# Kernel tuning notes

Measured on AMD Instinct MI355X. Metric: run time of the kernel, lower is better.

## Reference

```python
import jax, jax.numpy as jnp
import numpy as np

HEADS, DQK, DV = 4, 128, 128
HH, WW = 32, 32
SCALE = DQK ** -0.5
EPS = 1e-5


def bn(x, g, b, m, v):
    # eval-mode BatchNorm2d over channel dim of NCHW
    inv = g * jax.lax.rsqrt(v + EPS)
    return x * inv[:, None, None] + (b - m * inv)[:, None, None]


def rel_to_abs(x):
    # x: (B, Nh, L, 2L-1) -> (B, Nh, L, L)
    B, Nh, L, _ = x.shape
    x = jnp.pad(x, ((0, 0), (0, 0), (0, 0), (0, 1)))
    fx = x.reshape(B, Nh, L * 2 * L)
    fx = jnp.pad(fx, ((0, 0), (0, 0), (0, L - 1)))
    fx = fx.reshape(B, Nh, L + 1, 2 * L - 1)
    return fx[:, :, :L, L - 1:]


def rel_logits_1d(q, rel_k):
    # q: (B, Nh, H, W, D); rel_k: (2W-1, D)
    B, Nh, H, W, D = q.shape
    r = jnp.einsum('bnhwd,rd->bnhwr', q, rel_k)
    r = rel_to_abs(r.reshape(B, Nh * H, W, 2 * W - 1))
    r = r.reshape(B, Nh, H, W, W)
    return jnp.broadcast_to(r[:, :, :, None], (B, Nh, H, H, W, W))


def pos_bias(q, rel_h, rel_w):
    # q: (B, Nh, H*W, D), already scaled
    B, Nh, L, D = q.shape
    q5 = q.reshape(B, Nh, HH, WW, D)
    rw = rel_logits_1d(q5, rel_w)                     # (B,N,H,Hx,W,W)
    rw = rw.transpose(0, 1, 2, 4, 3, 5).reshape(B, Nh, HH * WW, HH * WW)
    rh = rel_logits_1d(q5.transpose(0, 1, 3, 2, 4), rel_h)  # (B,N,W,Wx,H,H)
    rh = rh.transpose(0, 1, 4, 2, 5, 3).reshape(B, Nh, HH * WW, HH * WW)
    return rw + rh


def to_heads(x):
    # (B, Nh*d, H, W) -> (B, Nh, H*W, d)
    B, C, H, W = x.shape
    x = x.reshape(B, HEADS, C // HEADS, H, W)
    return x.transpose(0, 1, 3, 4, 2).reshape(B, HEADS, H * W, C // HEADS)


def mhsa(x, w_qk, w_v, rel_h, rel_w):
    B, C, H, W = x.shape
    qk = jnp.einsum('bchw,oc->bohw', x, w_qk)
    q, k = jnp.split(qk, 2, axis=1)
    v = jnp.einsum('bchw,oc->bohw', x, w_v)
    q, k, v = to_heads(q), to_heads(k), to_heads(v)
    q = q * SCALE
    logits = jnp.einsum('bnid,bnjd->bnij', q, k) + pos_bias(q, rel_h, rel_w)
    weights = jax.nn.softmax(logits, axis=-1)
    out = jnp.einsum('bnij,bnjd->bnid', weights, v)   # (B,Nh,HW,dv)
    out = out.reshape(B, HEADS, H, W, DV).transpose(0, 1, 4, 2, 3)
    return out.reshape(B, HEADS * DV, H, W)


def setup_inputs() -> dict:
    key = jax.random.key(0)
    ks = jax.random.split(key, 12)
    d = {
        'x': jax.random.normal(ks[0], (8, 512, HH, WW), jnp.float32),
        'w_qk': jax.random.normal(ks[1], (2 * HEADS * DQK, 512), jnp.float32) * 0.02,
        'w_v': jax.random.normal(ks[2], (HEADS * DV, 512), jnp.float32) * 0.02,
        'rel_h': jax.random.normal(ks[3], (2 * HH - 1, DQK), jnp.float32) * SCALE,
        'rel_w': jax.random.normal(ks[4], (2 * WW - 1, DQK), jnp.float32) * SCALE,
        'g1': jnp.ones((512,), jnp.float32),
        'b1': jnp.zeros((512,), jnp.float32),
        'm1': jax.random.normal(ks[5], (512,), jnp.float32) * 0.1,
        'v1': jax.random.uniform(ks[6], (512,), jnp.float32) + 0.5,
        'g2': jnp.ones((512,), jnp.float32),
        'b2': jnp.zeros((512,), jnp.float32),
        'm2': jax.random.normal(ks[7], (512,), jnp.float32) * 0.1,
        'v2': jax.random.uniform(ks[8], (512,), jnp.float32) + 0.5,
        'w_fc': jax.random.normal(ks[9], (512, 512, 3, 3), jnp.float32) * 0.02,
        'bias_fc': jnp.zeros((512,), jnp.float32),
    }
    return d


def reference(x, w_qk, w_v, rel_h, rel_w, g1, b1, m1, v1, g2, b2, m2, v2, w_fc, bias_fc):
    out = jax.nn.relu(bn(x, g1, b1, m1, v1))
    out = mhsa(out, w_qk, w_v, rel_h, rel_w)
    x = out + x
    out = jax.nn.relu(bn(x, g2, b2, m2, v2))
    out = jax.lax.conv_general_dilated(
        out, w_fc, window_strides=(1, 1), padding='SAME',
        dimension_numbers=('NCHW', 'OIHW', 'NCHW')) + bias_fc[:, None, None]
    return out + x
```

## Files before the change

### kernel.cpp

```cpp
#include <hip/hip_runtime.h>

typedef __bf16 v8bf __attribute__((ext_vector_type(8)));
typedef float f32x4 __attribute__((ext_vector_type(4)));

#define DEVI static __device__ __forceinline__

DEVI v8bf load8(const __bf16* p) { return *reinterpret_cast<const v8bf*>(p); }

DEVI f32x4 mfma16(v8bf a, v8bf b, f32x4 c) {
  return __builtin_amdgcn_mfma_f32_16x16x32_bf16(a, b, c, 0, 0, 0);
}

DEVI void gld16(const __bf16* g, __bf16* l) {
  __builtin_amdgcn_global_load_lds(
      (const __attribute__((address_space(1))) unsigned int*)(const void*)g,
      (__attribute__((address_space(3))) unsigned int*)(void*)l, 16, 0, 0);
}

#define SCALE_Q 0.08838834764831845f

__global__ void k_prep(const float* __restrict__ wqk, const float* __restrict__ wv,
                       const float* __restrict__ relh, const float* __restrict__ relw,
                       const float* __restrict__ wfc, __bf16* __restrict__ wqkb,
                       __bf16* __restrict__ wvb, __bf16* __restrict__ rhb,
                       __bf16* __restrict__ rwb, __bf16* __restrict__ Wt,
                       float* __restrict__ zpad4) {
  const int bid = blockIdx.x, tid = threadIdx.x;
  if (bid < 2048) {
    int i = bid * 256 + tid;
    wqkb[i] = (__bf16)wqk[i];
  } else if (bid < 3072) {
    int i = (bid - 2048) * 256 + tid;
    wvb[i] = (__bf16)wv[i];
  } else if (bid < 3104) {
    int i = (bid - 3072) * 256 + tid;
    if (i < 8064) rhb[i] = (__bf16)relh[i];
  } else if (bid < 3136) {
    int i = (bid - 3104) * 256 + tid;
    if (i < 8064) rwb[i] = (__bf16)relw[i];
  } else if (bid < 4160) {
    int i = (bid - 3136) * 256 + tid;
    const float* src = wfc + (size_t)i * 9;
#pragma unroll
    for (int tap = 0; tap < 9; ++tap)
      Wt[(size_t)tap * 262144 + i] = (__bf16)src[tap];
  } else {
    int i = (bid - 4160) * 256 + tid;
    f32x4 z = {0.f, 0.f, 0.f, 0.f};
    reinterpret_cast<f32x4*>(zpad4)[i] = z;
  }
}

__global__ void k_bn1(const float* __restrict__ x, const float* __restrict__ g,
                      const float* __restrict__ bb, const float* __restrict__ m,
                      const float* __restrict__ v, __bf16* __restrict__ y) {
  __shared__ float tile[32][33];
  const int b = blockIdx.z, c0 = blockIdx.y * 32, s0 = blockIdx.x * 32;
  const int tx = threadIdx.x, ty = threadIdx.y;
#pragma unroll
  for (int r = 0; r < 4; ++r) {
    int c = c0 + ty + r * 8;
    float inv = g[c] * rsqrtf(v[c] + 1e-5f);
    float beta = bb[c] - m[c] * inv;
    float val = x[((size_t)b * 512 + c) * 1024 + s0 + tx] * inv + beta;
    tile[ty + r * 8][tx] = fmaxf(val, 0.0f);
  }
  __syncthreads();
#pragma unroll
  for (int r = 0; r < 4; ++r) {
    int s = s0 + ty + r * 8;
    y[((size_t)b * 1024 + s) * 512 + c0 + tx] = (__bf16)tile[tx][ty + r * 8];
  }
}

__global__ void k_bn2(const float* __restrict__ x2, const float* __restrict__ g,
                      const float* __restrict__ bb, const float* __restrict__ m,
                      const float* __restrict__ v, __bf16* __restrict__ zp) {
  __shared__ float tile[32][33];
  const int b = blockIdx.z, c0 = blockIdx.y * 32, s0 = blockIdx.x * 32;
  const int tx = threadIdx.x, ty = threadIdx.y;
#pragma unroll
  for (int r = 0; r < 4; ++r) {
    int c = c0 + ty + r * 8;
    float inv = g[c] * rsqrtf(v[c] + 1e-5f);
    float beta = bb[c] - m[c] * inv;
    float val = x2[((size_t)b * 512 + c) * 1024 + s0 + tx] * inv + beta;
    tile[ty + r * 8][tx] = fmaxf(val, 0.0f);
  }
  __syncthreads();
#pragma unroll
  for (int r = 0; r < 4; ++r) {
    int s = s0 + ty + r * 8;
    int hh = s >> 5, ww = s & 31;
    zp[(((size_t)b * 34 + hh + 1) * 34 + ww + 1) * 512 + c0 + tx] =
        (__bf16)tile[tx][ty + r * 8];
  }
}

__global__ __launch_bounds__(256) void k_proj(
    const __bf16* __restrict__ wall, const __bf16* __restrict__ y,
    __bf16* __restrict__ qout, __bf16* __restrict__ kout,
    __bf16* __restrict__ vout) {
  __shared__ __bf16 As[128 * 32];
  __shared__ __bf16 Bs[128 * 32];
  const int t = threadIdx.x;
  const int wave = t >> 6, lane = t & 63;
  const int l15 = lane & 15, quad = lane >> 4;
  const int mbase = blockIdx.x * 128;
  const int nbase = blockIdx.y * 128;
  const int mh = (wave >> 1) * 64, nh = (wave & 1) * 64;
  const bool isv = mbase >= 1024;

  const int row0 = t >> 2, part8 = (t & 3) * 8;
  const __bf16* gA0 = wall + (size_t)(mbase + row0) * 512 + part8;
  const __bf16* gA1 = gA0 + (size_t)64 * 512;
  const __bf16* gB0 = y + (size_t)(nbase + row0) * 512 + part8;
  const __bf16* gB1 = gB0 + (size_t)64 * 512;
  __bf16* lA0 = As + (size_t)(wave * 64) * 8;
  __bf16* lA1 = As + (size_t)(256 + wave * 64) * 8;
  __bf16* lB0 = Bs + (size_t)(wave * 64) * 8;
  __bf16* lB1 = Bs + (size_t)(256 + wave * 64) * 8;

  const f32x4 fz = {0.f, 0.f, 0.f, 0.f};
  f32x4 acc[4][4];
#pragma unroll
  for (int i = 0; i < 4; ++i)
#pragma unroll
    for (int j = 0; j < 4; ++j) acc[i][j] = fz;

  for (int k0 = 0; k0 < 512; k0 += 32) {
    __syncthreads();
    gld16(gA0 + k0, lA0);
    gld16(gA1 + k0, lA1);
    gld16(gB0 + k0, lB0);
    gld16(gB1 + k0, lB1);
    __syncthreads();
    v8bf a[4], bfr[4];
#pragma unroll
    for (int i = 0; i < 4; ++i)
      a[i] = load8(&As[(size_t)(mh + i * 16 + l15) * 32 + quad * 8]);
#pragma unroll
    for (int j = 0; j < 4; ++j)
      bfr[j] = load8(&Bs[(size_t)(nh + j * 16 + l15) * 32 + quad * 8]);
    if (isv) {
#pragma unroll
      for (int i = 0; i < 4; ++i)
#pragma unroll
        for (int j = 0; j < 4; ++j) acc[i][j] = mfma16(a[i], bfr[j], acc[i][j]);
    } else {
#pragma unroll
      for (int i = 0; i < 4; ++i)
#pragma unroll
        for (int j = 0; j < 4; ++j) acc[i][j] = mfma16(bfr[j], a[i], acc[i][j]);
    }
  }

  if (isv) {
#pragma unroll
    for (int i = 0; i < 4; ++i)
#pragma unroll
      for (int j = 0; j < 4; ++j)
#pragma unroll
        for (int r = 0; r < 4; ++r) {
          int o = mbase + mh + i * 16 + quad * 4 + r;
          int nflat = nbase + nh + j * 16 + l15;
          int b = nflat >> 10, s = nflat & 1023;
          int oe = o - 1024; int n = oe >> 7, d = oe & 127;
          vout[(((size_t)b * 4 + n) * 128 + d) * 1024 + s] = (__bf16)acc[i][j][r];
        }
  } else {
    const bool isq = mbase < 512;
#pragma unroll
    for (int i = 0; i < 4; ++i)
#pragma unroll
      for (int j = 0; j < 4; ++j)
#pragma unroll
        for (int r = 0; r < 4; ++r) {
          int o = mbase + mh + i * 16 + l15;
          int nflat = nbase + nh + j * 16 + quad * 4 + r;
          int b = nflat >> 10, s = nflat & 1023;
          float val = acc[i][j][r];
          if (isq) {
            int n = o >> 7, d = o & 127;
            qout[(((size_t)b * 4 + n) * 1024 + s) * 128 + d] = (__bf16)(val * SCALE_Q);
          } else {
            int oe = o - 512; int n = oe >> 7, d = oe & 127;
            kout[(((size_t)b * 4 + n) * 1024 + s) * 128 + d] = (__bf16)val;
          }
        }
  }
}

__global__ __launch_bounds__(256, 2) void k_attn(
    const __bf16* __restrict__ q, const __bf16* __restrict__ kmat,
    const __bf16* __restrict__ vt, const __bf16* __restrict__ relh,
    const __bf16* __restrict__ relw, const float* __restrict__ x,
    float* __restrict__ x2) {
  __shared__ __bf16 Ks[4 * 64 * 32];
  __shared__ __bf16 Vs[2 * 128 * 32];
  __shared__ __bf16 P[4 * 16 * 68];
  __shared__ __bf16 RWs[64][33];
  __shared__ __bf16 RHs[64][33];
  __shared__ float Lt[4][16];

  const int Lb = blockIdx.x;
  const int xcd = Lb & 7, local = Lb >> 3;
  const int bn = xcd * 4 + (local & 3);
  const int qblk = local >> 2;
  const int s0 = qblk * 64;

  const int t = threadIdx.x;
  const int wave = t >> 6, lane = t & 63;
  const int l15 = lane & 15, quad = lane >> 4;
  const size_t hoff = ((size_t)bn) << 17;
  const int s0w = s0 + wave * 16;
  const int wlo = (wave & 1) * 16;
  const int h0w = s0w >> 5;

  v8bf aq[4];
  {
    const __bf16* qp = q + hoff + (size_t)(s0w + l15) * 128;
#pragma unroll
    for (int kk = 0; kk < 4; ++kk) aq[kk] = load8(qp + kk * 32 + quad * 8);
  }

#pragma unroll
  for (int nt = 0; nt < 4; ++nt) {
    int rr = nt * 16 + l15;
    const __bf16* bp = relw + (size_t)rr * 128;
    f32x4 acc = {0.f, 0.f, 0.f, 0.f};
#pragma unroll
    for (int kk = 0; kk < 4; ++kk)
      acc = mfma16(aq[kk], load8(bp + kk * 32 + quad * 8), acc);
#pragma unroll
    for (int r = 0; r < 4; ++r) {
      int row = quad * 4 + r;
      int wj = rr + wlo + row - 31;
      if (wj >= 0 && wj < 32) RWs[wave * 16 + row][wj] = (__bf16)acc[r];
    }
  }
#pragma unroll
  for (int nt = 0; nt < 2; ++nt) {
    int hj = nt * 16 + l15;
    const __bf16* bp = relh + (size_t)(hj - h0w + 31) * 128;
    f32x4 acc = {0.f, 0.f, 0.f, 0.f};
#pragma unroll
    for (int kk = 0; kk < 4; ++kk)
      acc = mfma16(aq[kk], load8(bp + kk * 32 + quad * 8), acc);
#pragma unroll
    for (int r = 0; r < 4; ++r) RHs[wave * 16 + quad * 4 + r][hj] = (__bf16)acc[r];
  }

  const int row0 = t >> 2, part8 = (t & 3) * 8;
  const __bf16* kg = kmat + hoff + (size_t)row0 * 128 + part8;
  const __bf16* vg = vt + hoff + (size_t)row0 * 1024 + part8;
  __bf16* ksw = Ks + wave * 512;
  __bf16* vsw = Vs + wave * 512;

  const f32x4 fz = {0.f, 0.f, 0.f, 0.f};
  float lsum[4] = {0.f, 0.f, 0.f, 0.f};
  f32x4 oacc[8];
#pragma unroll
  for (int dt = 0; dt < 8; ++dt) oacc[dt] = fz;
  __bf16* Pw = P + wave * 16 * 68;

#pragma unroll 1
  for (int iter = 0; iter < 16; ++iter) {
    const int j0 = iter * 64;
    __syncthreads();
#pragma unroll
    for (int kk = 0; kk < 4; ++kk)
      gld16(kg + (size_t)j0 * 128 + kk * 32, ksw + kk * 2048);
#pragma unroll
    for (int kk2 = 0; kk2 < 2; ++kk2)
#pragma unroll
      for (int dh = 0; dh < 2; ++dh)
        gld16(vg + (size_t)dh * 64 * 1024 + j0 + kk2 * 32,
              vsw + kk2 * 4096 + dh * 2048);
    __syncthreads();

    f32x4 sacc[4];
#pragma unroll
    for (int nj = 0; nj < 4; ++nj) {
      f32x4 a = fz;
#pragma unroll
      for (int kk = 0; kk < 4; ++kk)
        a = mfma16(aq[kk],
                   load8(&Ks[kk * 2048 + (nj * 16 + l15) * 32 + quad * 8]), a);
      sacc[nj] = a;
    }
    const int hjb = j0 >> 5;
#pragma unroll
    for (int r = 0; r < 4; ++r) {
      const int row = quad * 4 + r;
      const int gi = wave * 16 + row;
      const float rw0 = (float)RWs[gi][l15], rw1 = (float)RWs[gi][l15 + 16];
      const float rh0 = (float)RHs[gi][hjb], rh1 = (float)RHs[gi][hjb + 1];
#pragma unroll
      for (int nj = 0; nj < 4; ++nj) {
        float val = sacc[nj][r] + ((nj & 1) ? rw1 : rw0) + ((nj & 2) ? rh1 : rh0);
        float p = __expf(fminf(val, 60.0f));
        lsum[r] += p;
        Pw[row * 68 + nj * 16 + l15] = (__bf16)p;
      }
    }
    v8bf pf[2];
#pragma unroll
    for (int kk2 = 0; kk2 < 2; ++kk2)
      pf[kk2] = *reinterpret_cast<const v8bf*>(&Pw[l15 * 68 + kk2 * 32 + quad * 8]);
#pragma unroll
    for (int dt = 0; dt < 8; ++dt) {
      f32x4 a = oacc[dt];
#pragma unroll
      for (int kk2 = 0; kk2 < 2; ++kk2)
        a = mfma16(load8(&Vs[kk2 * 4096 + (dt * 16 + l15) * 32 + quad * 8]),
                   pf[kk2], a);
      oacc[dt] = a;
    }
  }

#pragma unroll
  for (int r = 0; r < 4; ++r)
#pragma unroll
    for (int msk = 8; msk >= 1; msk >>= 1) lsum[r] += __shfl_xor(lsum[r], msk);
  if (l15 == 0) {
#pragma unroll
    for (int r = 0; r < 4; ++r) Lt[wave][quad * 4 + r] = lsum[r];
  }
  __syncthreads();

  {
    const float linv = 1.0f / Lt[wave][l15];
    const int s = s0w + l15;
#pragma unroll
    for (int dt = 0; dt < 8; ++dt)
#pragma unroll
      for (int r = 0; r < 4; ++r) {
        int d = dt * 16 + quad * 4 + r;
        size_t idx = ((size_t)bn * 128 + d) * 1024 + s;
        x2[idx] = oacc[dt][r] * linv + x[idx];
      }
  }
}

__global__ __launch_bounds__(256, 2) void k_conv(
    const __bf16* __restrict__ Wt, const __bf16* __restrict__ zp,
    float* __restrict__ part) {
  __shared__ __bf16 As[4 * 128 * 32];
  __shared__ __bf16 Bs[4 * 128 * 32];
  const int t = threadIdx.x;
  const int wave = t >> 6, lane = t & 63;
  const int l15 = lane & 15, quad = lane >> 4;

  const int id = blockIdx.x;
  const int combo = id & 7;
  const int ot = combo >> 1, sp = combo & 1;
  const int nt = id >> 3;
  const int mbase = ot * 128;
  const int nbase = nt * 128;
  const int cs = sp * 256;
  const int mh = (wave >> 1) * 64, nh = (wave & 1) * 64;

  const int row0 = t >> 2;
  const int part8 = (t & 3) * 8;
  const __bf16* gA0 = Wt + (size_t)(mbase + row0) * 512 + cs + part8;
  const __bf16* gA1 = gA0 + (size_t)64 * 512;
  const int n0 = nbase + row0;
  const int b0 = n0 >> 10, spn = n0 & 1023;
  const __bf16* gB0 =
      zp + ((size_t)(b0 * 34 + (spn >> 5) + 1) * 34 + (spn & 31) + 1) * 512 + cs + part8;
  const __bf16* gB1 = gB0 + (size_t)2 * 34 * 512;
  const int wofs = wave * 512;

  const f32x4 fz = {0.f, 0.f, 0.f, 0.f};
  f32x4 acc[4][4];
#pragma unroll
  for (int i = 0; i < 4; ++i)
#pragma unroll
    for (int j = 0; j < 4; ++j) acc[i][j] = fz;

#pragma unroll 1
  for (int tap = 0; tap < 9; ++tap) {
    const int dh = tap / 3 - 1, dw = tap % 3 - 1;
    const size_t aoff = (size_t)tap * 512 * 512;
    const int boff = (dh * 34 + dw) * 512;
#pragma unroll 1
    for (int k0 = 0; k0 < 256; k0 += 128) {
      __syncthreads();
#pragma unroll
      for (int c = 0; c < 4; ++c) {
        const int kq = k0 + c * 32;
        gld16(gA0 + aoff + kq, As + c * 4096 + wofs);
        gld16(gA1 + aoff + kq, As + c * 4096 + 2048 + wofs);
        gld16(gB0 + boff + kq, Bs + c * 4096 + wofs);
        gld16(gB1 + boff + kq, Bs + c * 4096 + 2048 + wofs);
      }
      __syncthreads();
#pragma unroll
      for (int c = 0; c < 4; ++c) {
        v8bf a[4], bfr[4];
#pragma unroll
        for (int i = 0; i < 4; ++i)
          a[i] = load8(&As[c * 4096 + (mh + i * 16 + l15) * 32 + quad * 8]);
#pragma unroll
        for (int j = 0; j < 4; ++j)
          bfr[j] = load8(&Bs[c * 4096 + (nh + j * 16 + l15) * 32 + quad * 8]);
#pragma unroll
        for (int i = 0; i < 4; ++i)
#pragma unroll
          for (int j = 0; j < 4; ++j) acc[i][j] = mfma16(a[i], bfr[j], acc[i][j]);
      }
    }
  }

  float* pout = part + (size_t)sp * 8 * 512 * 1024;
#pragma unroll
  for (int i = 0; i < 4; ++i)
#pragma unroll
    for (int j = 0; j < 4; ++j)
#pragma unroll
      for (int r = 0; r < 4; ++r) {
        int o = mbase + mh + i * 16 + quad * 4 + r;
        int nn = nbase + nh + j * 16 + l15;
        int bb2 = nn >> 10, s = nn & 1023;
        pout[((size_t)bb2 * 512 + o) * 1024 + s] = acc[i][j][r];
      }
}

__global__ void k_sum(const float* __restrict__ part, const float* __restrict__ bias,
                      const float* __restrict__ x2, float* __restrict__ out) {
  int i = blockIdx.x * 256 + threadIdx.x;
  int o = (i >> 8) & 511;
  f32x4 p0 = reinterpret_cast<const f32x4*>(part)[i];
  f32x4 p1 = reinterpret_cast<const f32x4*>(part + (size_t)8 * 512 * 1024)[i];
  f32x4 xr = reinterpret_cast<const f32x4*>(x2)[i];
  float bo = bias[o];
  f32x4 r;
#pragma unroll
  for (int c = 0; c < 4; ++c) r[c] = p0[c] + p1[c] + bo + xr[c];
  reinterpret_cast<f32x4*>(out)[i] = r;
}

extern "C" void kernel_launch(void* const* d_in, const int* in_sizes, int n_in,
                              void* d_out, int out_size, void* d_ws, size_t ws_size,
                              hipStream_t stream) {
  const float* x    = (const float*)d_in[0];
  const float* wqk  = (const float*)d_in[1];
  const float* wv   = (const float*)d_in[2];
  const float* relh = (const float*)d_in[3];
  const float* relw = (const float*)d_in[4];
  const float* g1   = (const float*)d_in[5];
  const float* b1   = (const float*)d_in[6];
  const float* m1   = (const float*)d_in[7];
  const float* v1   = (const float*)d_in[8];
  const float* g2   = (const float*)d_in[9];
  const float* b2   = (const float*)d_in[10];
  const float* m2   = (const float*)d_in[11];
  const float* v2   = (const float*)d_in[12];
  const float* wfc  = (const float*)d_in[13];
  const float* bfc  = (const float*)d_in[14];
  float* out = (float*)d_out;

  char* p = (char*)d_ws;
  __bf16* y    = (__bf16*)p; p += (size_t)8 * 1024 * 512 * 2;
  __bf16* qb   = (__bf16*)p; p += (size_t)8 * 4 * 1024 * 128 * 2;
  __bf16* kb   = (__bf16*)p; p += (size_t)8 * 4 * 1024 * 128 * 2;
  __bf16* vb   = (__bf16*)p; p += (size_t)8 * 4 * 1024 * 128 * 2;
  __bf16* Wt   = (__bf16*)p; p += (size_t)9 * 512 * 512 * 2;
  __bf16* wqkb = (__bf16*)p; p += (size_t)1024 * 512 * 2;
  __bf16* wvb  = (__bf16*)p; p += (size_t)512 * 512 * 2;
  __bf16* rhb  = (__bf16*)p; p += 32768;
  __bf16* rwb  = (__bf16*)p; p += 32768;
  float*  x2   = (float*)p;  p += (size_t)8 * 512 * 1024 * 4;
  __bf16* zpad = (__bf16*)p; p += (size_t)8 * 34 * 34 * 512 * 2;
  float* part = (float*)d_ws;

  k_prep<<<dim3(6472), dim3(256), 0, stream>>>(wqk, wv, relh, relw, wfc,
                                               wqkb, wvb, rhb, rwb, Wt, (float*)zpad);
  k_bn1<<<dim3(32, 16, 8), dim3(32, 8), 0, stream>>>(x, g1, b1, m1, v1, y);
  k_proj<<<dim3(12, 64), dim3(256), 0, stream>>>(wqkb, y, qb, kb, vb);
  k_attn<<<dim3(512), dim3(256), 0, stream>>>(qb, kb, vb, rhb, rwb, x, x2);
  k_bn2<<<dim3(32, 16, 8), dim3(32, 8), 0, stream>>>(x2, g2, b2, m2, v2, zpad);
  k_conv<<<dim3(512), dim3(256), 0, stream>>>(Wt, zpad, part);
  k_sum<<<dim3(4096), dim3(256), 0, stream>>>(part, bfc, x2, out);
}
```

Measured before the change: 238.9 us.

## Double-buffer K tiles and prefetch V to overlap loads with MFMA

Double-buffers the K tile in LDS and issues the next iteration's K load before the QK^T MFMAs. The next V tile is issued right after the PV MFMAs, and a vmcnt wait plus barrier replaces the old pair of syncthreads around each load, so global-to-LDS traffic overlaps compute. It also moves the relative-width bias into registers once, and raises wave priority around the MFMA blocks with s_setprio. The cost is an extra 16KB of LDS and hand-counted vmcnt logic, which could break if the load order changes.

```diff
diff --git a/kernel.cpp b/kernel.cpp
--- a/kernel.cpp
+++ b/kernel.cpp
@@ -196,7 +196,7 @@
     const __bf16* __restrict__ vt, const __bf16* __restrict__ relh,
     const __bf16* __restrict__ relw, const float* __restrict__ x,
     float* __restrict__ x2) {
-  __shared__ __bf16 Ks[4 * 64 * 32];
+  __shared__ __bf16 Ks[2][4 * 64 * 32];
   __shared__ __bf16 Vs[2 * 128 * 32];
   __shared__ __bf16 P[4 * 16 * 68];
   __shared__ __bf16 RWs[64][33];
@@ -217,6 +217,22 @@
   const int wlo = (wave & 1) * 16;
   const int h0w = s0w >> 5;
 
+  const int row0 = t >> 2, part8 = (t & 3) * 8;
+  const __bf16* kg = kmat + hoff + (size_t)row0 * 128 + part8;
+  const __bf16* vg = vt + hoff + (size_t)row0 * 1024 + part8;
+  __bf16* vsw = Vs + wave * 512;
+  __bf16* ksw0 = Ks[0] + wave * 512;
+  __bf16* ksw1 = Ks[1] + wave * 512;
+
+#pragma unroll
+  for (int kk2 = 0; kk2 < 2; ++kk2)
+#pragma unroll
+    for (int dh = 0; dh < 2; ++dh)
+      gld16(vg + (size_t)dh * 64 * 1024 + kk2 * 32, vsw + kk2 * 4096 + dh * 2048);
+#pragma unroll
+  for (int kk = 0; kk < 4; ++kk)
+    gld16(kg + kk * 32, ksw0 + kk * 2048);
+
   v8bf aq[4];
   {
     const __bf16* qp = q + hoff + (size_t)(s0w + l15) * 128;
@@ -251,11 +267,15 @@
     for (int r = 0; r < 4; ++r) RHs[wave * 16 + quad * 4 + r][hj] = (__bf16)acc[r];
   }
 
-  const int row0 = t >> 2, part8 = (t & 3) * 8;
-  const __bf16* kg = kmat + hoff + (size_t)row0 * 128 + part8;
-  const __bf16* vg = vt + hoff + (size_t)row0 * 1024 + part8;
-  __bf16* ksw = Ks + wave * 512;
-  __bf16* vsw = Vs + wave * 512;
+  __syncthreads();
+
+  float rwreg[4][2];
+#pragma unroll
+  for (int r = 0; r < 4; ++r) {
+    const int gi = wave * 16 + quad * 4 + r;
+    rwreg[r][0] = (float)RWs[gi][l15];
+    rwreg[r][1] = (float)RWs[gi][l15 + 16];
+  }
 
   const f32x4 fz = {0.f, 0.f, 0.f, 0.f};
   float lsum[4] = {0.f, 0.f, 0.f, 0.f};
@@ -266,35 +286,34 @@
 
 #pragma unroll 1
   for (int iter = 0; iter < 16; ++iter) {
-    const int j0 = iter * 64;
-    __syncthreads();
+    const int cur = iter & 1;
+    const __bf16* kcur = Ks[cur];
+    __bf16* knxt = cur ? ksw0 : ksw1;
+    const int jp = (iter < 15 ? iter + 1 : 15) * 64;
+
 #pragma unroll
     for (int kk = 0; kk < 4; ++kk)
-      gld16(kg + (size_t)j0 * 128 + kk * 32, ksw + kk * 2048);
-#pragma unroll
-    for (int kk2 = 0; kk2 < 2; ++kk2)
-#pragma unroll
-      for (int dh = 0; dh < 2; ++dh)
-        gld16(vg + (size_t)dh * 64 * 1024 + j0 + kk2 * 32,
-              vsw + kk2 * 4096 + dh * 2048);
-    __syncthreads();
+      gld16(kg + (size_t)jp * 128 + kk * 32, knxt + kk * 2048);
 
     f32x4 sacc[4];
+    __builtin_amdgcn_s_setprio(1);
 #pragma unroll
     for (int nj = 0; nj < 4; ++nj) {
       f32x4 a = fz;
 #pragma unroll
       for (int kk = 0; kk < 4; ++kk)
         a = mfma16(aq[kk],
-                   load8(&Ks[kk * 2048 + (nj * 16 + l15) * 32 + quad * 8]), a);
+                   load8(&kcur[kk * 2048 + (nj * 16 + l15) * 32 + quad * 8]), a);
       sacc[nj] = a;
     }
-    const int hjb = j0 >> 5;
+    __builtin_amdgcn_s_setprio(0);
+
+    const int hjb = iter * 2;
 #pragma unroll
     for (int r = 0; r < 4; ++r) {
       const int row = quad * 4 + r;
       const int gi = wave * 16 + row;
-      const float rw0 = (float)RWs[gi][l15], rw1 = (float)RWs[gi][l15 + 16];
+      const float rw0 = rwreg[r][0], rw1 = rwreg[r][1];
       const float rh0 = (float)RHs[gi][hjb], rh1 = (float)RHs[gi][hjb + 1];
 #pragma unroll
       for (int nj = 0; nj < 4; ++nj) {
@@ -308,6 +327,12 @@
 #pragma unroll
     for (int kk2 = 0; kk2 < 2; ++kk2)
       pf[kk2] = *reinterpret_cast<const v8bf*>(&Pw[l15 * 68 + kk2 * 32 + quad * 8]);
+
+    asm volatile("s_waitcnt vmcnt(4)" ::: "memory");
+    __builtin_amdgcn_s_barrier();
+    __builtin_amdgcn_sched_barrier(0);
+
+    __builtin_amdgcn_s_setprio(1);
 #pragma unroll
     for (int dt = 0; dt < 8; ++dt) {
       f32x4 a = oacc[dt];
@@ -317,6 +342,16 @@
                    pf[kk2], a);
       oacc[dt] = a;
     }
+    __builtin_amdgcn_s_setprio(0);
+
+    __syncthreads();
+
+#pragma unroll
+    for (int kk2 = 0; kk2 < 2; ++kk2)
+#pragma unroll
+      for (int dh = 0; dh < 2; ++dh)
+        gld16(vg + (size_t)dh * 64 * 1024 + jp + kk2 * 32,
+              vsw + kk2 * 4096 + dh * 2048);
   }
 
 #pragma unroll
```

New measurement: 238.8 us. About the same (-0.1%).
